# Optimization experiments

Measured on AMD Instinct MI355X. Metric: run time of the kernel, lower is better.

## Reference

```python
import jax, jax.numpy as jnp
import numpy as np

C = 128
PC = 6
NH = 8
HD = C // NH
EPS = 1e-5


def _layernorm(x, g, b):
    m = jnp.mean(x, axis=-1, keepdims=True)
    v = jnp.mean((x - m) ** 2, axis=-1, keepdims=True)
    return (x - m) * jax.lax.rsqrt(v + EPS) * g + b


def setup_inputs() -> dict:
    key = jax.random.key(0)
    ks = jax.random.split(key, 16)
    s = 0.02
    inp = {
        "x": jax.random.normal(ks[0], (2, C, 32, 64, 64), dtype=jnp.float32),
        "polar_coords": jax.random.normal(ks[1], (2, PC, 32, 64, 64), dtype=jnp.float32),
        "Wq": jax.random.normal(ks[2], (C, C), dtype=jnp.float32) * s,
        "bq": jnp.zeros((C,), jnp.float32),
        "Wk": jax.random.normal(ks[3], (C, C), dtype=jnp.float32) * s,
        "bk": jnp.zeros((C,), jnp.float32),
        "Wv": jax.random.normal(ks[4], (C, C), dtype=jnp.float32) * s,
        "bv": jnp.zeros((C,), jnp.float32),
        "Wp": jax.random.normal(ks[5], (PC, C), dtype=jnp.float32) * s,
        "bp": jnp.zeros((C,), jnp.float32),
        "Wo": jax.random.normal(ks[6], (C, C), dtype=jnp.float32) * s,
        "bo": jnp.zeros((C,), jnp.float32),
        "g1": jnp.ones((C,), jnp.float32),
        "beta1": jnp.zeros((C,), jnp.float32),
        "g2": jnp.ones((C,), jnp.float32),
        "beta2": jnp.zeros((C,), jnp.float32),
        "W1": jax.random.normal(ks[7], (C, 4 * C), dtype=jnp.float32) * s,
        "bf1": jnp.zeros((4 * C,), jnp.float32),
        "W2": jax.random.normal(ks[8], (4 * C, C), dtype=jnp.float32) * s,
        "bf2": jnp.zeros((C,), jnp.float32),
    }
    return inp


def reference(x, polar_coords, Wq, bq, Wk, bk, Wv, bv, Wp, bp, Wo, bo,
              g1, beta1, g2, beta2, W1, bf1, W2, bf2):
    B, Cc, D, H, W = x.shape
    N = B * D * H * W
    # [B,C,D,H,W] -> [N,C]
    x_flat = jnp.transpose(x, (0, 2, 3, 4, 1)).reshape(N, Cc)
    polar_flat = jnp.transpose(polar_coords, (0, 2, 3, 4, 1)).reshape(N, -1)

    x_with_polar = x_flat + polar_flat @ Wp + bp
    residual = x_with_polar
    x_norm = _layernorm(x_with_polar, g1, beta1)

    Q = (x_norm @ Wq + bq).reshape(N, NH, HD)
    K = (x_norm @ Wk + bk).reshape(N, NH, HD)
    V = (x_norm @ Wv + bv).reshape(N, NH, HD)

    # tiny per-token cross-head attention: scores [N, NH, NH]
    scores = jnp.einsum('nhd,ngd->nhg', Q, K) / np.float32(np.sqrt(HD))
    attn = jax.nn.softmax(scores, axis=-1)
    attended = jnp.einsum('nhg,ngd->nhd', attn, V).reshape(N, Cc)

    out = attended @ Wo + bo + residual
    residual2 = out
    h = _layernorm(out, g2, beta2)
    h = jax.nn.relu(h @ W1 + bf1) @ W2 + bf2
    out = h + residual2

    out = out.reshape(B, D, H, W, Cc)
    return jnp.transpose(out, (0, 4, 1, 2, 3))
```

## Files before the change

kernel.cpp:

```cpp
#include <hip/hip_runtime.h>

typedef unsigned short u16;
typedef float f32x4 __attribute__((ext_vector_type(4)));
typedef short bf16x8 __attribute__((ext_vector_type(8)));

#define DHW 131072
#define OFF_WQ 0
#define OFF_WK 16384
#define OFF_WV 32768
#define OFF_WO 49152
#define OFF_W1 65536
#define OFF_W2 131072

__device__ __forceinline__ float b2f(u16 u){ union{unsigned i; float f;} x; x.i=((unsigned)u)<<16; return x.f; }
__device__ __forceinline__ u16 f2b(float f){ union{float f; unsigned u;} x; x.f=f; unsigned r=x.u+0x7fffu+((x.u>>16)&1u); return (u16)(r>>16); }
__device__ __forceinline__ int cofs(int tok, int cch){ return (tok<<7) + ((((cch>>3) ^ (tok&7)))<<3) + (cch&7); }

__global__ void pack_w(const float* __restrict__ Wq, const float* __restrict__ Wk,
                       const float* __restrict__ Wv, const float* __restrict__ Wo,
                       const float* __restrict__ W1, const float* __restrict__ W2,
                       u16* __restrict__ ws){
  int tid = blockIdx.x*256 + threadIdx.x;
  const float* src; int dst, K, N, fb;
  if      (tid <  2048){ src=Wq; dst=OFF_WQ; K=128; N=128; fb=tid;       }
  else if (tid <  4096){ src=Wk; dst=OFF_WK; K=128; N=128; fb=tid-2048;  }
  else if (tid <  6144){ src=Wv; dst=OFF_WV; K=128; N=128; fb=tid-4096;  }
  else if (tid <  8192){ src=Wo; dst=OFF_WO; K=128; N=128; fb=tid-6144;  }
  else if (tid < 16384){ src=W1; dst=OFF_W1; K=128; N=512; fb=tid-8192;  }
  else                 { src=W2; dst=OFF_W2; K=512; N=128; fb=tid-16384; }
  int l = fb & 63, f = fb >> 6;
  int ksc = K >> 5;
  int nt = f / ksc, ks = f - nt*ksc;
  int k0 = ks*32 + ((l>>4)<<3);
  int col = nt*16 + (l&15);
  union { uint4 v; u16 u[8]; } pk;
  #pragma unroll
  for (int j=0;j<8;j++) pk.u[j] = f2b(src[(k0+j)*N + col]);
  *reinterpret_cast<uint4*>(ws + dst + f*512 + l*8) = pk.v;
}

__device__ __forceinline__ void zacc(f32x4 (&a)[4][2]){
  #pragma unroll
  for (int i=0;i<4;i++){ a[i][0]=(f32x4){0.f,0.f,0.f,0.f}; a[i][1]=(f32x4){0.f,0.f,0.f,0.f}; }
}
__device__ __forceinline__ void mmT(const u16* __restrict__ act, const u16* __restrict__ wf,
                                    int ctb, int ksc, int ks0, int l, f32x4 (&acc)[4][2]){
  #pragma unroll
  for (int ks=0; ks<4; ++ks){
    bf16x8 w0 = *(const bf16x8*)(wf + ((ctb+0)*ksc + ks0+ks)*512 + l*8);
    bf16x8 w1 = *(const bf16x8*)(wf + ((ctb+1)*ksc + ks0+ks)*512 + l*8);
    int g = ks*4 + (l>>4);
    #pragma unroll
    for (int tt=0; tt<4; ++tt){
      int tok = tt*16 + (l&15);
      bf16x8 a = *(const bf16x8*)(act + (tok<<7) + ((g ^ (tok&7))<<3));
      acc[tt][0] = __builtin_amdgcn_mfma_f32_16x16x32_bf16(w0, a, acc[tt][0], 0,0,0);
      acc[tt][1] = __builtin_amdgcn_mfma_f32_16x16x32_bf16(w1, a, acc[tt][1], 0,0,0);
    }
  }
}
__device__ __forceinline__ void packT(ushort4 (&pk)[4][2], const f32x4 (&acc)[4][2],
                                      const u16* __restrict__ bias, int ctb, int l, bool relu){
  #pragma unroll
  for (int cw=0; cw<2; ++cw){
    int cch = (ctb+cw)*16 + ((l>>4)<<2);
    float b0=b2f(bias[cch]), b1=b2f(bias[cch+1]), b2v=b2f(bias[cch+2]), b3=b2f(bias[cch+3]);
    #pragma unroll
    for (int tt=0; tt<4; ++tt){
      float v0=acc[tt][cw][0]+b0, v1=acc[tt][cw][1]+b1, v2=acc[tt][cw][2]+b2v, v3=acc[tt][cw][3]+b3;
      if (relu){ v0=fmaxf(v0,0.f); v1=fmaxf(v1,0.f); v2=fmaxf(v2,0.f); v3=fmaxf(v3,0.f); }
      pk[tt][cw] = (ushort4){ f2b(v0), f2b(v1), f2b(v2), f2b(v3) };
    }
  }
}
__device__ __forceinline__ void storePK(u16* dst, const ushort4 (&pk)[4][2], int ctb, int l){
  #pragma unroll
  for (int cw=0; cw<2; ++cw){
    int cch = ((ctb+cw)*16 + ((l>>4)<<2)) & 127;
    #pragma unroll
    for (int tt=0; tt<4; ++tt){
      int tok = tt*16 + (l&15);
      *(ushort4*)&dst[cofs(tok,cch)] = pk[tt][cw];
    }
  }
}
__device__ __forceinline__ void load16(const u16* buf, int t, int c0, float* o){
  int g = c0 >> 3;
  union { uint4 v; u16 u[8]; } a, b;
  a.v = *(const uint4*)&buf[(t<<7) + (( g    ^ (t&7))<<3)];
  b.v = *(const uint4*)&buf[(t<<7) + (((g+1) ^ (t&7))<<3)];
  #pragma unroll
  for (int j=0;j<8;j++){ o[j]=b2f(a.u[j]); o[8+j]=b2f(b.u[j]); }
}

__global__ __launch_bounds__(256,4) void fused(
    const float* __restrict__ x, const float* __restrict__ pol,
    const float* __restrict__ Wp, const u16* __restrict__ ws,
    const float* __restrict__ bp, const float* __restrict__ bq,
    const float* __restrict__ bk, const float* __restrict__ bv,
    const float* __restrict__ bo, const float* __restrict__ bf1,
    const float* __restrict__ bf2, const float* __restrict__ g1,
    const float* __restrict__ be1, const float* __restrict__ g2,
    const float* __restrict__ be2, float* __restrict__ out)
{
  __shared__ __align__(16) unsigned char arena[40448];
  u16*   bufA = (u16*)  (arena);
  u16*   bufB = (u16*)  (arena + 16384);
  float* red   = (float*)(arena + 32768);
  float* stats = (float*)(arena + 34816);
  u16*   par   = (u16*)  (arena + 35328);

  const int tid = threadIdx.x;
  const int t   = tid & 63;
  const int p   = __builtin_amdgcn_readfirstlane(tid >> 6);
  const int l   = t;

  for (int i=tid; i<2560; i+=256){
    float v;
    if      (i< 128) v = bp [i];
    else if (i< 256) v = g1 [i-128];
    else if (i< 384) v = be1[i-256];
    else if (i< 512) v = g2 [i-384];
    else if (i< 640) v = be2[i-512];
    else if (i<1408) v = Wp [i-640];
    else if (i<1536) v = bq [i-1408];
    else if (i<1664) v = bk [i-1536];
    else if (i<1792) v = bv [i-1664];
    else if (i<1920) v = bo [i-1792];
    else if (i<2048) v = bf2[i-1920];
    else             v = bf1[i-2048];
    par[i] = f2b(v);
  }
  const int bi   = (int)((blockIdx.x*64) >> 17);
  const int dhw0 = (int)((blockIdx.x*64) & (DHW-1));
  const float* xb = x   + (size_t)bi*128*DHW + dhw0;
  const float* pb = pol + (size_t)bi*6*DHW + dhw0;
  float pl6[6];
  #pragma unroll
  for (int j=0;j<6;j++) pl6[j] = pb[(size_t)j*DHW + t];
  __syncthreads();

  float xp[32]; float s1=0.f, s2=0.f;
  #pragma unroll
  for (int it=0; it<32; ++it){
    int c = p*32 + it;
    float a = xb[(size_t)c*DHW + t] + b2f(par[c]);
    #pragma unroll
    for (int j=0;j<6;j++) a = fmaf(pl6[j], b2f(par[640 + j*128 + c]), a);
    xp[it]=a; s1+=a; s2+=a*a;
  }
  #pragma unroll
  for (int cl=0; cl<4; ++cl){
    union { uint4 v; u16 u[8]; } pk;
    #pragma unroll
    for (int j=0;j<8;j++) pk.u[j]=f2b(xp[cl*8+j]);
    *(uint4*)&bufB[(t<<7) + (((p*4+cl) ^ (t&7))<<3)] = pk.v;
  }
  red[p*64+t]=s1; red[256+p*64+t]=s2;
  __syncthreads();
  if (tid < 64){
    float a=0.f,b=0.f;
    #pragma unroll
    for (int i=0;i<4;i++){ a+=red[i*64+tid]; b+=red[256+i*64+tid]; }
    float m=a*0.0078125f, v=b*0.0078125f-m*m;
    stats[tid*2]=m; stats[tid*2+1]=rsqrtf(v+1e-5f);
  }
  __syncthreads();

  {
    float mn=stats[t*2], rs=stats[t*2+1];
    #pragma unroll
    for (int cl=0; cl<4; ++cl){
      union { uint4 v; u16 u[8]; } pk;
      #pragma unroll
      for (int j=0;j<8;j++){ int c=p*32+cl*8+j; pk.u[j]=f2b((xp[cl*8+j]-mn)*rs*b2f(par[128+c])+b2f(par[256+c])); }
      *(uint4*)&bufA[(t<<7) + (((p*4+cl) ^ (t&7))<<3)] = pk.v;
    }
  }
  ushort4 resq[4][2];
  #pragma unroll
  for (int cw=0; cw<2; ++cw){
    int cch = (p*2+cw)*16 + ((l>>4)<<2);
    #pragma unroll
    for (int tt=0; tt<4; ++tt) resq[tt][cw] = *(const ushort4*)&bufB[cofs(tt*16+(l&15), cch)];
  }
  __syncthreads();

  f32x4 acc[4][2]; ushort4 pkt[4][2];
  zacc(acc); mmT(bufA, ws+OFF_WQ, p*2, 4, 0, l, acc);
  packT(pkt, acc, par+1408, p*2, l, false); storePK(bufB, pkt, p*2, l);
  ushort4 pkV[4][2];
  zacc(acc); mmT(bufA, ws+OFF_WV, p*2, 4, 0, l, acc);
  packT(pkV, acc, par+1664, p*2, l, false);
  zacc(acc); mmT(bufA, ws+OFF_WK, p*2, 4, 0, l, acc);
  __syncthreads();
  packT(pkt, acc, par+1536, p*2, l, false); storePK(bufA, pkt, p*2, l);
  __syncthreads();

  float sc[16];
  {
    float qv[32];
    load16(bufB, t, p*32, qv); load16(bufB, t, p*32+16, qv+16);
    #pragma unroll
    for (int g8=0; g8<8; ++g8){
      float kv[16]; load16(bufA, t, g8*16, kv);
      float d0=0.f,d1=0.f;
      #pragma unroll
      for (int d=0; d<16; ++d){ d0=fmaf(qv[d],kv[d],d0); d1=fmaf(qv[16+d],kv[d],d1); }
      sc[g8]=d0*0.25f; sc[8+g8]=d1*0.25f;
    }
    #pragma unroll
    for (int hh=0; hh<2; ++hh){
      float mx = sc[hh*8];
      #pragma unroll
      for (int g8=1; g8<8; ++g8) mx = fmaxf(mx, sc[hh*8+g8]);
      float sm=0.f;
      #pragma unroll
      for (int g8=0; g8<8; ++g8){ float e=__expf(sc[hh*8+g8]-mx); sc[hh*8+g8]=e; sm+=e; }
      float inv = 1.f/sm;
      #pragma unroll
      for (int g8=0; g8<8; ++g8) sc[hh*8+g8]*=inv;
    }
  }
  __syncthreads();
  storePK(bufA, pkV, p*2, l);
  __syncthreads();
  {
    float ov[32];
    #pragma unroll
    for (int i=0;i<32;i++) ov[i]=0.f;
    #pragma unroll
    for (int g8=0; g8<8; ++g8){
      float vv[16]; load16(bufA, t, g8*16, vv);
      #pragma unroll
      for (int d=0; d<16; ++d){ ov[d]=fmaf(sc[g8],vv[d],ov[d]); ov[16+d]=fmaf(sc[8+g8],vv[d],ov[16+d]); }
    }
    #pragma unroll
    for (int cl=0; cl<4; ++cl){
      union { uint4 v; u16 u[8]; } pk;
      #pragma unroll
      for (int j=0;j<8;j++) pk.u[j]=f2b(ov[cl*8+j]);
      *(uint4*)&bufB[(t<<7) + (((p*4+cl) ^ (t&7))<<3)] = pk.v;
    }
  }
  __syncthreads();

  ushort4 res2q[4][2];
  zacc(acc); mmT(bufB, ws+OFF_WO, p*2, 4, 0, l, acc);
  #pragma unroll
  for (int cw=0; cw<2; ++cw){
    int cch = (p*2+cw)*16 + ((l>>4)<<2);
    float b0=b2f(par[1792+cch]), b1=b2f(par[1793+cch]), b2v=b2f(par[1794+cch]), b3=b2f(par[1795+cch]);
    #pragma unroll
    for (int tt=0; tt<4; ++tt){
      int tok = tt*16 + (l&15);
      ushort4 r4 = resq[tt][cw];
      ushort4 pk = (ushort4){ f2b(acc[tt][cw][0]+b0+b2f(r4.x)),
                              f2b(acc[tt][cw][1]+b1+b2f(r4.y)),
                              f2b(acc[tt][cw][2]+b2v+b2f(r4.z)),
                              f2b(acc[tt][cw][3]+b3+b2f(r4.w)) };
      res2q[tt][cw] = pk;
      *(ushort4*)&bufA[cofs(tok,cch)] = pk;
    }
  }
  __syncthreads();

  float ovl[32]; s1=0.f; s2=0.f;
  #pragma unroll
  for (int cl=0; cl<4; ++cl){
    union { uint4 v; u16 u[8]; } pk;
    pk.v = *(const uint4*)&bufA[(t<<7) + (((p*4+cl) ^ (t&7))<<3)];
    #pragma unroll
    for (int j=0;j<8;j++){ float v=b2f(pk.u[j]); ovl[cl*8+j]=v; s1+=v; s2+=v*v; }
  }
  red[p*64+t]=s1; red[256+p*64+t]=s2;
  __syncthreads();
  if (tid < 64){
    float a=0.f,b=0.f;
    #pragma unroll
    for (int i=0;i<4;i++){ a+=red[i*64+tid]; b+=red[256+i*64+tid]; }
    float m=a*0.0078125f, v=b*0.0078125f-m*m;
    stats[tid*2]=m; stats[tid*2+1]=rsqrtf(v+1e-5f);
  }
  __syncthreads();
  {
    float mn=stats[t*2], rs=stats[t*2+1];
    #pragma unroll
    for (int cl=0; cl<4; ++cl){
      union { uint4 v; u16 u[8]; } pk;
      #pragma unroll
      for (int j=0;j<8;j++){ int c=p*32+cl*8+j; pk.u[j]=f2b((ovl[cl*8+j]-mn)*rs*b2f(par[384+c])+b2f(par[512+c])); }
      *(uint4*)&bufB[(t<<7) + (((p*4+cl) ^ (t&7))<<3)] = pk.v;
    }
  }
  __syncthreads();

  f32x4 acc2[4][2]; zacc(acc2);
  #pragma unroll 1
  for (int ch=0; ch<4; ++ch){
    f32x4 acc1[4][2]; zacc(acc1);
    mmT(bufB, ws+OFF_W1, ch*8+p*2, 4, 0, l, acc1);
    packT(pkt, acc1, par+2048, ch*8+p*2, l, true); storePK(bufA, pkt, ch*8+p*2, l);
    __syncthreads();
    mmT(bufA, ws+OFF_W2, p*2, 16, ch*4, l, acc2);
    __syncthreads();
  }

  float* ob = out + (size_t)bi*128*DHW + dhw0;
  #pragma unroll
  for (int cw=0; cw<2; ++cw){
    int cch = (p*2+cw)*16 + ((l>>4)<<2);
    float b0=b2f(par[1920+cch]), b1=b2f(par[1921+cch]), b2v=b2f(par[1922+cch]), b3=b2f(par[1923+cch]);
    #pragma unroll
    for (int tt=0; tt<4; ++tt){
      int tok = tt*16 + (l&15);
      ushort4 r4 = res2q[tt][cw];
      ob[(size_t)(cch+0)*DHW + tok] = acc2[tt][cw][0] + b0 + b2f(r4.x);
      ob[(size_t)(cch+1)*DHW + tok] = acc2[tt][cw][1] + b1 + b2f(r4.y);
      ob[(size_t)(cch+2)*DHW + tok] = acc2[tt][cw][2] + b2v + b2f(r4.z);
      ob[(size_t)(cch+3)*DHW + tok] = acc2[tt][cw][3] + b3 + b2f(r4.w);
    }
  }
}

extern "C" void kernel_launch(void* const* d_in, const int* in_sizes, int n_in,
                              void* d_out, int out_size, void* d_ws, size_t ws_size,
                              hipStream_t stream){
  const float* x   = (const float*)d_in[0];
  const float* pol = (const float*)d_in[1];
  const float* Wq  = (const float*)d_in[2];
  const float* bq  = (const float*)d_in[3];
  const float* Wk  = (const float*)d_in[4];
  const float* bk  = (const float*)d_in[5];
  const float* Wv  = (const float*)d_in[6];
  const float* bv  = (const float*)d_in[7];
  const float* Wp  = (const float*)d_in[8];
  const float* bp  = (const float*)d_in[9];
  const float* Wo  = (const float*)d_in[10];
  const float* bo  = (const float*)d_in[11];
  const float* g1  = (const float*)d_in[12];
  const float* be1 = (const float*)d_in[13];
  const float* g2  = (const float*)d_in[14];
  const float* be2 = (const float*)d_in[15];
  const float* W1  = (const float*)d_in[16];
  const float* bf1 = (const float*)d_in[17];
  const float* W2  = (const float*)d_in[18];
  const float* bf2 = (const float*)d_in[19];
  u16* ws = (u16*)d_ws;
  pack_w<<<96, 256, 0, stream>>>(Wq, Wk, Wv, Wo, W1, W2, ws);
  fused<<<4096, 256, 0, stream>>>(x, pol, Wp, ws, bp, bq, bk, bv, bo, bf1, bf2,
                                  g1, be1, g2, be2, (float*)d_out);
}
```

Before: 470.6 us.

## Switch GEMMs to 32x32x16 MFMA tiles with packed bf16 conversion and fp32 params

Replaces the 16x16x32 MFMA tiling with 32x32x16 MFMA, so each wave computes a 32-token by 64-channel tile instead of 64 by 32. The weight pre-pack layout and all pack/store/epilogue index math change to match. It also uses the hardware v_cvt_pk_bf16_f32 instruction for float-to-bf16 packing and keeps parameters in LDS as fp32 rather than bf16. The goal is fewer MFMA issues and activation LDS reads, plus cheaper conversions, at the cost of more LDS and a lower occupancy hint (launch bounds 4 to 3).

```diff
diff --git a/kernel.cpp b/kernel.cpp
--- a/kernel.cpp
+++ b/kernel.cpp
@@ -1,7 +1,7 @@
 #include <hip/hip_runtime.h>
 
 typedef unsigned short u16;
-typedef float f32x4 __attribute__((ext_vector_type(4)));
+typedef float f32x16 __attribute__((ext_vector_type(16)));
 typedef short bf16x8 __attribute__((ext_vector_type(8)));
 
 #define DHW 131072
@@ -14,7 +14,12 @@
 
 __device__ __forceinline__ float b2f(u16 u){ union{unsigned i; float f;} x; x.i=((unsigned)u)<<16; return x.f; }
 __device__ __forceinline__ u16 f2b(float f){ union{float f; unsigned u;} x; x.f=f; unsigned r=x.u+0x7fffu+((x.u>>16)&1u); return (u16)(r>>16); }
-__device__ __forceinline__ int cofs(int tok, int cch){ return (tok<<7) + ((((cch>>3) ^ (tok&7)))<<3) + (cch&7); }
+__device__ __forceinline__ unsigned pk2bf(float lo, float hi){
+  unsigned r; asm("v_cvt_pk_bf16_f32 %0, %1, %2" : "=v"(r) : "v"(lo), "v"(hi)); return r;
+}
+__device__ __forceinline__ float lo2f(unsigned u){ union{unsigned i; float f;} x; x.i=u<<16; return x.f; }
+__device__ __forceinline__ float hi2f(unsigned u){ union{unsigned i; float f;} x; x.i=u&0xffff0000u; return x.f; }
+__device__ __forceinline__ int cofs(int tok, int c){ return (tok<<7) + ((((c>>3) ^ (tok&7)))<<3) + (c&7); }
 
 __global__ void pack_w(const float* __restrict__ Wq, const float* __restrict__ Wk,
                        const float* __restrict__ Wv, const float* __restrict__ Wo,
@@ -29,59 +34,53 @@
   else if (tid < 16384){ src=W1; dst=OFF_W1; K=128; N=512; fb=tid-8192;  }
   else                 { src=W2; dst=OFF_W2; K=512; N=128; fb=tid-16384; }
   int l = fb & 63, f = fb >> 6;
-  int ksc = K >> 5;
-  int nt = f / ksc, ks = f - nt*ksc;
-  int k0 = ks*32 + ((l>>4)<<3);
-  int col = nt*16 + (l&15);
+  int ksc = K >> 4;
+  int ct = f / ksc, ks = f - ct*ksc;
+  int k0 = ks*16 + ((l>>5)<<3);
+  int col = ct*32 + (l&31);
   union { uint4 v; u16 u[8]; } pk;
   #pragma unroll
   for (int j=0;j<8;j++) pk.u[j] = f2b(src[(k0+j)*N + col]);
   *reinterpret_cast<uint4*>(ws + dst + f*512 + l*8) = pk.v;
 }
 
-__device__ __forceinline__ void zacc(f32x4 (&a)[4][2]){
-  #pragma unroll
-  for (int i=0;i<4;i++){ a[i][0]=(f32x4){0.f,0.f,0.f,0.f}; a[i][1]=(f32x4){0.f,0.f,0.f,0.f}; }
-}
-__device__ __forceinline__ void mmT(const u16* __restrict__ act, const u16* __restrict__ wf,
-                                    int ctb, int ksc, int ks0, int l, f32x4 (&acc)[4][2]){
-  #pragma unroll
-  for (int ks=0; ks<4; ++ks){
-    bf16x8 w0 = *(const bf16x8*)(wf + ((ctb+0)*ksc + ks0+ks)*512 + l*8);
-    bf16x8 w1 = *(const bf16x8*)(wf + ((ctb+1)*ksc + ks0+ks)*512 + l*8);
-    int g = ks*4 + (l>>4);
-    #pragma unroll
-    for (int tt=0; tt<4; ++tt){
-      int tok = tt*16 + (l&15);
-      bf16x8 a = *(const bf16x8*)(act + (tok<<7) + ((g ^ (tok&7))<<3));
-      acc[tt][0] = __builtin_amdgcn_mfma_f32_16x16x32_bf16(w0, a, acc[tt][0], 0,0,0);
-      acc[tt][1] = __builtin_amdgcn_mfma_f32_16x16x32_bf16(w1, a, acc[tt][1], 0,0,0);
-    }
-  }
-}
-__device__ __forceinline__ void packT(ushort4 (&pk)[4][2], const f32x4 (&acc)[4][2],
-                                      const u16* __restrict__ bias, int ctb, int l, bool relu){
-  #pragma unroll
-  for (int cw=0; cw<2; ++cw){
-    int cch = (ctb+cw)*16 + ((l>>4)<<2);
-    float b0=b2f(bias[cch]), b1=b2f(bias[cch+1]), b2v=b2f(bias[cch+2]), b3=b2f(bias[cch+3]);
-    #pragma unroll
-    for (int tt=0; tt<4; ++tt){
-      float v0=acc[tt][cw][0]+b0, v1=acc[tt][cw][1]+b1, v2=acc[tt][cw][2]+b2v, v3=acc[tt][cw][3]+b3;
-      if (relu){ v0=fmaxf(v0,0.f); v1=fmaxf(v1,0.f); v2=fmaxf(v2,0.f); v3=fmaxf(v3,0.f); }
-      pk[tt][cw] = (ushort4){ f2b(v0), f2b(v1), f2b(v2), f2b(v3) };
-    }
-  }
-}
-__device__ __forceinline__ void storePK(u16* dst, const ushort4 (&pk)[4][2], int ctb, int l){
-  #pragma unroll
-  for (int cw=0; cw<2; ++cw){
-    int cch = ((ctb+cw)*16 + ((l>>4)<<2)) & 127;
-    #pragma unroll
-    for (int tt=0; tt<4; ++tt){
-      int tok = tt*16 + (l&15);
-      *(ushort4*)&dst[cofs(tok,cch)] = pk[tt][cw];
-    }
+__device__ __forceinline__ f32x16 z16(){ f32x16 z; 
+  #pragma unroll
+  for(int i=0;i<16;i++) z[i]=0.f; return z; }
+
+__device__ __forceinline__ void mm32(const u16* __restrict__ act, const u16* __restrict__ wf,
+                                     int cb, int ksc, int ks0, int tok, int hi, int l,
+                                     f32x16 (&acc)[2]){
+  #pragma unroll
+  for (int kst=0; kst<8; ++kst){
+    int g = kst*2 + hi;
+    bf16x8 a  = *(const bf16x8*)(act + (tok<<7) + ((g ^ (tok&7))<<3));
+    bf16x8 w0 = *(const bf16x8*)(wf + ((cb+0)*ksc + ks0+kst)*512 + l*8);
+    bf16x8 w1 = *(const bf16x8*)(wf + ((cb+1)*ksc + ks0+kst)*512 + l*8);
+    acc[0] = __builtin_amdgcn_mfma_f32_32x32x16_bf16(w0, a, acc[0], 0,0,0);
+    acc[1] = __builtin_amdgcn_mfma_f32_32x32x16_bf16(w1, a, acc[1], 0,0,0);
+  }
+}
+__device__ __forceinline__ void packT32(uint2 (&pk)[2][4], const f32x16 (&acc)[2],
+                                        const float* __restrict__ bias, int cbase, int hi, bool relu){
+  #pragma unroll
+  for (int cw=0;cw<2;cw++)
+  #pragma unroll
+  for (int q=0;q<4;q++){
+    int c0 = cbase + cw*32 + 4*hi + 8*q;
+    float v0=acc[cw][q*4+0]+bias[c0],   v1=acc[cw][q*4+1]+bias[c0+1],
+          v2=acc[cw][q*4+2]+bias[c0+2], v3=acc[cw][q*4+3]+bias[c0+3];
+    if(relu){v0=fmaxf(v0,0.f);v1=fmaxf(v1,0.f);v2=fmaxf(v2,0.f);v3=fmaxf(v3,0.f);}
+    pk[cw][q]=(uint2){pk2bf(v0,v1),pk2bf(v2,v3)};
+  }
+}
+__device__ __forceinline__ void store32(u16* dst, const uint2 (&pk)[2][4], int cbase, int tok, int hi){
+  #pragma unroll
+  for (int cw=0;cw<2;cw++)
+  #pragma unroll
+  for (int q=0;q<4;q++){
+    int c0 = (cbase + cw*32 + 4*hi + 8*q) & 127;
+    *(uint2*)&dst[cofs(tok,c0)] = pk[cw][q];
   }
 }
 __device__ __forceinline__ void load16(const u16* buf, int t, int c0, float* o){
@@ -93,7 +92,7 @@
   for (int j=0;j<8;j++){ o[j]=b2f(a.u[j]); o[8+j]=b2f(b.u[j]); }
 }
 
-__global__ __launch_bounds__(256,4) void fused(
+__global__ __launch_bounds__(256,3) void fused(
     const float* __restrict__ x, const float* __restrict__ pol,
     const float* __restrict__ Wp, const u16* __restrict__ ws,
     const float* __restrict__ bp, const float* __restrict__ bq,
@@ -103,17 +102,21 @@
     const float* __restrict__ be1, const float* __restrict__ g2,
     const float* __restrict__ be2, float* __restrict__ out)
 {
-  __shared__ __align__(16) unsigned char arena[40448];
+  __shared__ __align__(16) unsigned char arena[45568];
   u16*   bufA = (u16*)  (arena);
   u16*   bufB = (u16*)  (arena + 16384);
   float* red   = (float*)(arena + 32768);
   float* stats = (float*)(arena + 34816);
-  u16*   par   = (u16*)  (arena + 35328);
+  float* parf  = (float*)(arena + 35328);
 
   const int tid = threadIdx.x;
   const int t   = tid & 63;
   const int p   = __builtin_amdgcn_readfirstlane(tid >> 6);
   const int l   = t;
+  const int hi    = l >> 5;
+  const int tok   = (p&1)*32 + (l&31);
+  const int cbase = (p>>1)*64;
+  const int cb2   = (p>>1)*2;
 
   for (int i=tid; i<2560; i+=256){
     float v;
@@ -129,7 +132,7 @@
     else if (i<1920) v = bo [i-1792];
     else if (i<2048) v = bf2[i-1920];
     else             v = bf1[i-2048];
-    par[i] = f2b(v);
+    parf[i] = v;
   }
   const int bi   = (int)((blockIdx.x*64) >> 17);
   const int dhw0 = (int)((blockIdx.x*64) & (DHW-1));
@@ -144,17 +147,16 @@
   #pragma unroll
   for (int it=0; it<32; ++it){
     int c = p*32 + it;
-    float a = xb[(size_t)c*DHW + t] + b2f(par[c]);
-    #pragma unroll
-    for (int j=0;j<6;j++) a = fmaf(pl6[j], b2f(par[640 + j*128 + c]), a);
+    float a = xb[(size_t)c*DHW + t] + parf[c];
+    #pragma unroll
+    for (int j=0;j<6;j++) a = fmaf(pl6[j], parf[640 + j*128 + c], a);
     xp[it]=a; s1+=a; s2+=a*a;
   }
   #pragma unroll
   for (int cl=0; cl<4; ++cl){
-    union { uint4 v; u16 u[8]; } pk;
-    #pragma unroll
-    for (int j=0;j<8;j++) pk.u[j]=f2b(xp[cl*8+j]);
-    *(uint4*)&bufB[(t<<7) + (((p*4+cl) ^ (t&7))<<3)] = pk.v;
+    uint4 pk = (uint4){ pk2bf(xp[cl*8+0],xp[cl*8+1]), pk2bf(xp[cl*8+2],xp[cl*8+3]),
+                        pk2bf(xp[cl*8+4],xp[cl*8+5]), pk2bf(xp[cl*8+6],xp[cl*8+7]) };
+    *(uint4*)&bufB[(t<<7) + (((p*4+cl) ^ (t&7))<<3)] = pk;
   }
   red[p*64+t]=s1; red[256+p*64+t]=s2;
   __syncthreads();
@@ -171,30 +173,37 @@
     float mn=stats[t*2], rs=stats[t*2+1];
     #pragma unroll
     for (int cl=0; cl<4; ++cl){
-      union { uint4 v; u16 u[8]; } pk;
-      #pragma unroll
-      for (int j=0;j<8;j++){ int c=p*32+cl*8+j; pk.u[j]=f2b((xp[cl*8+j]-mn)*rs*b2f(par[128+c])+b2f(par[256+c])); }
-      *(uint4*)&bufA[(t<<7) + (((p*4+cl) ^ (t&7))<<3)] = pk.v;
-    }
-  }
-  ushort4 resq[4][2];
-  #pragma unroll
-  for (int cw=0; cw<2; ++cw){
-    int cch = (p*2+cw)*16 + ((l>>4)<<2);
-    #pragma unroll
-    for (int tt=0; tt<4; ++tt) resq[tt][cw] = *(const ushort4*)&bufB[cofs(tt*16+(l&15), cch)];
-  }
-  __syncthreads();
-
-  f32x4 acc[4][2]; ushort4 pkt[4][2];
-  zacc(acc); mmT(bufA, ws+OFF_WQ, p*2, 4, 0, l, acc);
-  packT(pkt, acc, par+1408, p*2, l, false); storePK(bufB, pkt, p*2, l);
-  ushort4 pkV[4][2];
-  zacc(acc); mmT(bufA, ws+OFF_WV, p*2, 4, 0, l, acc);
-  packT(pkV, acc, par+1664, p*2, l, false);
-  zacc(acc); mmT(bufA, ws+OFF_WK, p*2, 4, 0, l, acc);
-  __syncthreads();
-  packT(pkt, acc, par+1536, p*2, l, false); storePK(bufA, pkt, p*2, l);
+      float y[8];
+      #pragma unroll
+      for (int j=0;j<8;j++){ int c=p*32+cl*8+j; y[j]=(xp[cl*8+j]-mn)*rs*parf[128+c]+parf[256+c]; }
+      uint4 pk = (uint4){ pk2bf(y[0],y[1]), pk2bf(y[2],y[3]), pk2bf(y[4],y[5]), pk2bf(y[6],y[7]) };
+      *(uint4*)&bufA[(t<<7) + (((p*4+cl) ^ (t&7))<<3)] = pk;
+    }
+  }
+  uint2 resq[2][4];
+  #pragma unroll
+  for (int cw=0;cw<2;cw++)
+  #pragma unroll
+  for (int q=0;q<4;q++){
+    int c0 = cbase + cw*32 + 4*hi + 8*q;
+    resq[cw][q] = *(const uint2*)&bufB[cofs(tok,c0)];
+  }
+  __syncthreads();
+
+  uint2 pkt[2][4], pkV[2][4];
+  {
+    f32x16 acc[2];
+    acc[0]=z16(); acc[1]=z16();
+    mm32(bufA, ws+OFF_WQ, cb2, 8, 0, tok, hi, l, acc);
+    packT32(pkt, acc, parf+1408, cbase, hi, false); store32(bufB, pkt, cbase, tok, hi);
+    acc[0]=z16(); acc[1]=z16();
+    mm32(bufA, ws+OFF_WV, cb2, 8, 0, tok, hi, l, acc);
+    packT32(pkV, acc, parf+1664, cbase, hi, false);
+    acc[0]=z16(); acc[1]=z16();
+    mm32(bufA, ws+OFF_WK, cb2, 8, 0, tok, hi, l, acc);
+    __syncthreads();
+    packT32(pkt, acc, parf+1536, cbase, hi, false); store32(bufA, pkt, cbase, tok, hi);
+  }
   __syncthreads();
 
   float sc[16];
@@ -223,7 +232,7 @@
     }
   }
   __syncthreads();
-  storePK(bufA, pkV, p*2, l);
+  store32(bufA, pkV, cbase, tok, hi);
   __syncthreads();
   {
     float ov[32];
@@ -237,30 +246,31 @@
     }
     #pragma unroll
     for (int cl=0; cl<4; ++cl){
-      union { uint4 v; u16 u[8]; } pk;
-      #pragma unroll
-      for (int j=0;j<8;j++) pk.u[j]=f2b(ov[cl*8+j]);
-      *(uint4*)&bufB[(t<<7) + (((p*4+cl) ^ (t&7))<<3)] = pk.v;
-    }
-  }
-  __syncthreads();
-
-  ushort4 res2q[4][2];
-  zacc(acc); mmT(bufB, ws+OFF_WO, p*2, 4, 0, l, acc);
-  #pragma unroll
-  for (int cw=0; cw<2; ++cw){
-    int cch = (p*2+cw)*16 + ((l>>4)<<2);
-    float b0=b2f(par[1792+cch]), b1=b2f(par[1793+cch]), b2v=b2f(par[1794+cch]), b3=b2f(par[1795+cch]);
-    #pragma unroll
-    for (int tt=0; tt<4; ++tt){
-      int tok = tt*16 + (l&15);
-      ushort4 r4 = resq[tt][cw];
-      ushort4 pk = (ushort4){ f2b(acc[tt][cw][0]+b0+b2f(r4.x)),
-                              f2b(acc[tt][cw][1]+b1+b2f(r4.y)),
-                              f2b(acc[tt][cw][2]+b2v+b2f(r4.z)),
-                              f2b(acc[tt][cw][3]+b3+b2f(r4.w)) };
-      res2q[tt][cw] = pk;
-      *(ushort4*)&bufA[cofs(tok,cch)] = pk;
+      uint4 pk = (uint4){ pk2bf(ov[cl*8+0],ov[cl*8+1]), pk2bf(ov[cl*8+2],ov[cl*8+3]),
+                          pk2bf(ov[cl*8+4],ov[cl*8+5]), pk2bf(ov[cl*8+6],ov[cl*8+7]) };
+      *(uint4*)&bufB[(t<<7) + (((p*4+cl) ^ (t&7))<<3)] = pk;
+    }
+  }
+  __syncthreads();
+
+  uint2 res2q[2][4];
+  {
+    f32x16 acc[2];
+    acc[0]=z16(); acc[1]=z16();
+    mm32(bufB, ws+OFF_WO, cb2, 8, 0, tok, hi, l, acc);
+    #pragma unroll
+    for (int cw=0;cw<2;cw++)
+    #pragma unroll
+    for (int q=0;q<4;q++){
+      int c0 = cbase + cw*32 + 4*hi + 8*q;
+      uint2 r = resq[cw][q];
+      float v0 = acc[cw][q*4+0]+parf[1792+c0]  +lo2f(r.x);
+      float v1 = acc[cw][q*4+1]+parf[1793+c0]  +hi2f(r.x);
+      float v2 = acc[cw][q*4+2]+parf[1794+c0]  +lo2f(r.y);
+      float v3 = acc[cw][q*4+3]+parf[1795+c0]  +hi2f(r.y);
+      uint2 pk = (uint2){ pk2bf(v0,v1), pk2bf(v2,v3) };
+      res2q[cw][q] = pk;
+      *(uint2*)&bufA[cofs(tok,c0)] = pk;
     }
   }
   __syncthreads();
@@ -287,39 +297,37 @@
     float mn=stats[t*2], rs=stats[t*2+1];
     #pragma unroll
     for (int cl=0; cl<4; ++cl){
-      union { uint4 v; u16 u[8]; } pk;
-      #pragma unroll
-      for (int j=0;j<8;j++){ int c=p*32+cl*8+j; pk.u[j]=f2b((ovl[cl*8+j]-mn)*rs*b2f(par[384+c])+b2f(par[512+c])); }
-      *(uint4*)&bufB[(t<<7) + (((p*4+cl) ^ (t&7))<<3)] = pk.v;
-    }
-  }
-  __syncthreads();
-
-  f32x4 acc2[4][2]; zacc(acc2);
+      float y[8];
+      #pragma unroll
+      for (int j=0;j<8;j++){ int c=p*32+cl*8+j; y[j]=(ovl[cl*8+j]-mn)*rs*parf[384+c]+parf[512+c]; }
+      uint4 pk = (uint4){ pk2bf(y[0],y[1]), pk2bf(y[2],y[3]), pk2bf(y[4],y[5]), pk2bf(y[6],y[7]) };
+      *(uint4*)&bufB[(t<<7) + (((p*4+cl) ^ (t&7))<<3)] = pk;
+    }
+  }
+  __syncthreads();
+
+  f32x16 acc2[2]; acc2[0]=z16(); acc2[1]=z16();
   #pragma unroll 1
   for (int ch=0; ch<4; ++ch){
-    f32x4 acc1[4][2]; zacc(acc1);
-    mmT(bufB, ws+OFF_W1, ch*8+p*2, 4, 0, l, acc1);
-    packT(pkt, acc1, par+2048, ch*8+p*2, l, true); storePK(bufA, pkt, ch*8+p*2, l);
+    f32x16 acc1[2]; acc1[0]=z16(); acc1[1]=z16();
+    mm32(bufB, ws+OFF_W1, ch*4+cb2, 8, 0, tok, hi, l, acc1);
+    packT32(pkt, acc1, parf+2048+ch*128, cbase, hi, true); store32(bufA, pkt, cbase, tok, hi);
     __syncthreads();
-    mmT(bufA, ws+OFF_W2, p*2, 16, ch*4, l, acc2);
+    mm32(bufA, ws+OFF_W2, cb2, 32, ch*8, tok, hi, l, acc2);
     __syncthreads();
   }
 
   float* ob = out + (size_t)bi*128*DHW + dhw0;
   #pragma unroll
-  for (int cw=0; cw<2; ++cw){
-    int cch = (p*2+cw)*16 + ((l>>4)<<2);
-    float b0=b2f(par[1920+cch]), b1=b2f(par[1921+cch]), b2v=b2f(par[1922+cch]), b3=b2f(par[1923+cch]);
-    #pragma unroll
-    for (int tt=0; tt<4; ++tt){
-      int tok = tt*16 + (l&15);
-      ushort4 r4 = res2q[tt][cw];
-      ob[(size_t)(cch+0)*DHW + tok] = acc2[tt][cw][0] + b0 + b2f(r4.x);
-      ob[(size_t)(cch+1)*DHW + tok] = acc2[tt][cw][1] + b1 + b2f(r4.y);
-      ob[(size_t)(cch+2)*DHW + tok] = acc2[tt][cw][2] + b2v + b2f(r4.z);
-      ob[(size_t)(cch+3)*DHW + tok] = acc2[tt][cw][3] + b3 + b2f(r4.w);
-    }
+  for (int cw=0;cw<2;cw++)
+  #pragma unroll
+  for (int q=0;q<4;q++){
+    int c0 = cbase + cw*32 + 4*hi + 8*q;
+    uint2 r = res2q[cw][q];
+    ob[(size_t)(c0+0)*DHW + tok] = acc2[cw][q*4+0] + parf[1920+c0]   + lo2f(r.x);
+    ob[(size_t)(c0+1)*DHW + tok] = acc2[cw][q*4+1] + parf[1921+c0]   + hi2f(r.x);
+    ob[(size_t)(c0+2)*DHW + tok] = acc2[cw][q*4+2] + parf[1922+c0]   + lo2f(r.y);
+    ob[(size_t)(c0+3)*DHW + tok] = acc2[cw][q*4+3] + parf[1923+c0]   + hi2f(r.y);
   }
 }
 
```

Measured after the change: 488.2 us. +3.8%, slower.
